# Kernel optimization log

Measured on AMD Instinct MI355X. Metric: run time of the kernel, lower is better.

Reference implementation:

```python
import jax, jax.numpy as jnp
import numpy as np

B, N, D, KNN = 2, 2048, 512, 16
F = 4 * D  # ffn hidden
LN_EPS = 1e-6  # flax LayerNorm default


def _ln(x, s, b):
    m = jnp.mean(x, axis=-1, keepdims=True)
    v = jnp.var(x, axis=-1, keepdims=True)
    return s * (x - m) * jax.lax.rsqrt(v + LN_EPS) + b


def _mobius_add(x, y, c):
    x2 = jnp.sum(x * x, axis=-1, keepdims=True)
    y2 = jnp.sum(y * y, axis=-1, keepdims=True)
    xy = jnp.sum(x * y, axis=-1, keepdims=True)
    num = (1 + 2 * c * xy + c * y2) * x + (1 - c * x2) * y
    den = 1 + 2 * c * xy + c * c * x2 * y2
    return num / jnp.clip(den, 1e-8, None)


def _logmap0(y, c):
    sqrt_c = jnp.sqrt(c)
    y_norm = jnp.clip(jnp.linalg.norm(y, axis=-1, keepdims=True), 1e-8, None)
    arg = jnp.minimum(sqrt_c * y_norm, 1.0 - 1e-7)
    return 1.0 / (sqrt_c * y_norm) * jnp.arctanh(arg) * y


def setup_inputs() -> dict:
    key = jax.random.key(0)
    ks = jax.random.split(key, 8)
    w = lambda k, shape: 0.02 * jax.random.normal(k, shape, dtype=jnp.float32)
    z = lambda *shape: jnp.zeros(shape, jnp.float32)
    o = lambda *shape: jnp.ones(shape, jnp.float32)
    return {
        'x': jax.random.normal(ks[0], (B, N, D), jnp.float32),
        'positions': 0.02 * jax.random.normal(ks[1], (B, N, D), jnp.float32),  # inside Poincare ball
        'c': jnp.ones((), jnp.float32),
        'Wq': w(ks[2], (D, D)), 'bq': z(D),
        'Wk': w(ks[3], (D, D)), 'bk': z(D),
        'Wv': w(ks[4], (D, D)), 'bv': z(D),
        'Wo': w(ks[5], (D, D)), 'bo': z(D),
        'W1': w(ks[6], (D, F)), 'b1': z(F),
        'W2': w(ks[7], (F, D)), 'b2': z(D),
        'ln1_s': o(D), 'ln1_b': z(D),
        'ln2_s': o(D), 'ln2_b': z(D),
        'geo_s': o(D), 'geo_b': z(D),
        'align_scale': o(1), 'feat_scale': o(1),
    }


def reference(x, positions, c, Wq, bq, Wk, bk, Wv, bv, Wo, bo, W1, b1, W2, b2,
              ln1_s, ln1_b, ln2_s, ln2_b, geo_s, geo_b, align_scale, feat_scale):
    b_, n_, d_ = x.shape
    x_res = x
    xn = _ln(x, ln1_s, ln1_b)
    q = xn @ Wq + bq
    kk = xn @ Wk + bk
    v = xn @ Wv + bv

    # Poincare distance matrix [B, N, N] (expanded ||x-y||^2 to avoid [B,N,N,D] intermediate)
    p2 = jnp.sum(positions * positions, axis=-1)            # [B, N]
    ip = jnp.einsum('bid,bjd->bij', positions, positions)   # [B, N, N]
    diff_sq = jnp.maximum(p2[:, :, None] + p2[:, None, :] - 2.0 * ip, 0.0)
    den = (1 - c * p2)[:, :, None] * (1 - c * p2)[:, None, :]
    arg = 1 + 2 * c * diff_sq / jnp.clip(den, 1e-8, None)
    dist = jnp.arccosh(jnp.maximum(arg, 1.0 + 1e-7)) / jnp.sqrt(c)

    _, idx = jax.lax.top_k(-dist, KNN)                      # [B, N, K]
    bix = jnp.arange(b_)[:, None, None]

    key_pos = positions[bix, idx]                           # [B, N, K, D]
    query_pos = positions[:, :, None, :]                    # [B, N, 1, D]
    geo = _logmap0(_mobius_add(-query_pos, key_pos, c), c)  # [B, N, K, D]
    geo = _ln(geo, geo_s, geo_b)

    gk = kk[bix, idx]                                       # [B, N, K, D]
    gv = v[bix, idx]                                        # [B, N, K, D]

    align = jnp.einsum('bnd,bnkd->bnk', q, geo)
    feat = jnp.einsum('bnd,bnkd->bnk', q, gk)
    scores = feat_scale * feat + align_scale * align
    w = jax.nn.softmax(scores, axis=-1)
    attn = jnp.einsum('bnk,bnkd->bnd', w, gv)

    x1 = x_res + attn @ Wo + bo
    h = _ln(x1, ln2_s, ln2_b)
    out = x1 + jax.nn.gelu(h @ W1 + b1) @ W2 + b2
    return out
```

## Files before the change

kernel.cpp:

```cpp
#include <hip/hip_runtime.h>
#include <hip/hip_bf16.h>
#include <math.h>

#define NTOK 2048
#define DDIM 512
#define FDIM 2048
#define KNN_K 16
#define ROWS 4096

typedef __hip_bfloat16 hb;
typedef unsigned long long ull;
typedef short s8v __attribute__((ext_vector_type(8)));
typedef short s4v __attribute__((ext_vector_type(4)));
typedef float f4v __attribute__((ext_vector_type(4)));

__device__ __forceinline__ float b2f(hb h) { return __bfloat162float(h); }
__device__ __forceinline__ float bits2f(short s) {
    return __uint_as_float(((unsigned int)(unsigned short)s) << 16);
}

__device__ __forceinline__ float ldin(const void* p, size_t i, int f32m) {
    return f32m ? ((const float*)p)[i] : b2f(((const hb*)p)[i]);
}
__device__ __forceinline__ float ld_scalar(const void* p, int f32m) {
    return f32m ? *(const float*)p : b2f(*(const hb*)p);
}
__device__ __forceinline__ short f2bs(float v) {
    hb h = __float2bfloat16(v);
    short s; __builtin_memcpy(&s, &h, 2); return s;
}
__device__ __forceinline__ short hb2s(hb h) {
    short s; __builtin_memcpy(&s, &h, 2); return s;
}

__device__ __forceinline__ void ld8(const void* p, size_t base, int fm, float* o) {
    if (fm) {
        f4v a = *(const f4v*)((const float*)p + base);
        f4v b = *(const f4v*)((const float*)p + base + 4);
        o[0]=a[0]; o[1]=a[1]; o[2]=a[2]; o[3]=a[3];
        o[4]=b[0]; o[5]=b[1]; o[6]=b[2]; o[7]=b[3];
    } else {
        s8v v = *(const s8v*)((const hb*)p + base);
        #pragma unroll
        for (int e = 0; e < 8; ++e) o[e] = bits2f(v[e]);
    }
}

__device__ __forceinline__ int detect_fm(const void* x) {
    const unsigned short* u = (const unsigned short*)x;
    const int lane = threadIdx.x & 63;
    int bad = 0;
    #pragma unroll
    for (int t = 0; t < 16; ++t) {
        unsigned short h = u[lane * 16 + t];
        int e = (h >> 7) & 0xFF;
        if (e == 0xFF) bad++;
        else if (e >= 0x8E) bad++;
        else if (e != 0 && e <= 0x66) bad++;
    }
    #pragma unroll
    for (int off = 1; off < 64; off <<= 1) bad += __shfl_xor(bad, off);
    return bad > 100 ? 1 : 0;
}

__device__ __forceinline__ ull shfl_xor_u64(ull x, int mask) {
    unsigned lo = (unsigned)x, hi = (unsigned)(x >> 32);
    lo = __shfl_xor(lo, mask); hi = __shfl_xor(hi, mask);
    return ((ull)hi << 32) | lo;
}

__device__ __forceinline__ float gelu_f(float x) {
    float u = 1.5957691216057308f * x * (1.f + 0.044715f * x * x);
    return x / (1.f + __expf(-u));
}

__device__ __forceinline__ void tr_tile(const void* src, hb* dst, int K, int N,
                                        int k0, int n0, int fm) {
    __shared__ float t[32][33];
    const int tx = threadIdx.x & 31, ty = threadIdx.x >> 5;
    #pragma unroll
    for (int r = 0; r < 32; r += 8)
        t[ty + r][tx] = ldin(src, (size_t)(k0 + ty + r) * N + n0 + tx, fm);
    __syncthreads();
    #pragma unroll
    for (int r = 0; r < 32; r += 8)
        dst[(size_t)(n0 + ty + r) * K + k0 + tx] = __float2bfloat16(t[tx][ty + r]);
}

__global__ void setup_kernel(const void* __restrict__ pos, const void* __restrict__ x,
                             const void* __restrict__ ln1s, const void* __restrict__ ln1b,
                             const void* __restrict__ Wq, const void* __restrict__ Wk,
                             const void* __restrict__ Wv, const void* __restrict__ Wo,
                             const void* __restrict__ W1, const void* __restrict__ W2,
                             hb* __restrict__ ph, hb* __restrict__ pl,
                             float* __restrict__ p2, float* __restrict__ spos,
                             hb* __restrict__ xnB,
                             hb* __restrict__ WqkvT, hb* __restrict__ WoT,
                             hb* __restrict__ W1T, hb* __restrict__ W2T,
                             int* __restrict__ fmflag) {
    const int fm = detect_fm(x);
    const int bx = blockIdx.x;
    if (bx == 0 && threadIdx.x == 0) *fmflag = fm;
    if (bx < 1024) {
        const int seg = bx >> 8, t = bx & 255;
        const int n0 = (t & 15) * 32, k0 = (t >> 4) * 32;
        const void* src = (seg == 0) ? Wq : (seg == 1) ? Wk : (seg == 2) ? Wv : Wo;
        hb* dst = (seg == 3) ? WoT : (WqkvT + (size_t)seg * 512 * 512);
        tr_tile(src, dst, 512, 512, k0, n0, fm);
    } else if (bx < 3072) {
        const int b = bx - 1024;
        if (b < 1024) {
            const int n0 = (b & 63) * 32, k0 = (b >> 6) * 32;
            tr_tile(W1, W1T, 512, 2048, k0, n0, fm);
        } else {
            const int b2 = b - 1024;
            const int n0 = (b2 & 15) * 32, k0 = (b2 >> 4) * 32;
            tr_tile(W2, W2T, 2048, 512, k0, n0, fm);
        }
    } else {
        const int idx = bx - 3072;
        const int lane = threadIdx.x & 63, wv = threadIdx.x >> 6;
        const int row = idx * 4 + wv;
        const int d0 = lane * 8;
        float pv[8], xv[8];
        ld8(pos, (size_t)row * DDIM + d0, fm, pv);
        ld8(x,   (size_t)row * DDIM + d0, fm, xv);
        s8v phv, plv;
        float s2 = 0.f, s1 = 0.f, sum = 0.f, sq = 0.f;
        #pragma unroll
        for (int e = 0; e < 8; ++e) {
            float v = pv[e];
            hb h = __float2bfloat16(v);
            phv[e] = hb2s(h);
            plv[e] = f2bs(v - b2f(h));
            s2 += v * v; s1 += v;
            sum += xv[e]; sq += xv[e] * xv[e];
        }
        *(s8v*)(ph + (size_t)row * DDIM + d0) = phv;
        *(s8v*)(pl + (size_t)row * DDIM + d0) = plv;
        #pragma unroll
        for (int off = 32; off; off >>= 1) {
            s2 += __shfl_down(s2, off); s1 += __shfl_down(s1, off);
            sum += __shfl_down(sum, off); sq += __shfl_down(sq, off);
        }
        if (lane == 0) { p2[row] = s2; spos[row] = s1; }
        const float ts = __shfl(sum, 0), tq = __shfl(sq, 0);
        const float mean = ts * (1.f / DDIM);
        const float var = tq * (1.f / DDIM) - mean * mean;
        const float rstd = rsqrtf(var + 1e-6f);
        float sv[8], bv2[8];
        ld8(ln1s, d0, fm, sv);
        ld8(ln1b, d0, fm, bv2);
        s8v xo;
        #pragma unroll
        for (int e = 0; e < 8; ++e)
            xo[e] = f2bs(sv[e] * (xv[e] - mean) * rstd + bv2[e]);
        *(s8v*)(xnB + (size_t)row * DDIM + d0) = xo;
    }
}

__global__ void ln_kernel(const float* __restrict__ xin,
                          const void* __restrict__ s, const void* __restrict__ b,
                          hb* __restrict__ y, const int* __restrict__ fmflag) {
    const int m = *fmflag;
    const int lane = threadIdx.x & 63, wv = threadIdx.x >> 6;
    const int row = blockIdx.x * 4 + wv;
    const int d0 = lane * 8;
    const float* xp = xin + (size_t)row * DDIM + d0;
    f4v a = *(const f4v*)xp, c4 = *(const f4v*)(xp + 4);
    float v[8] = {a[0], a[1], a[2], a[3], c4[0], c4[1], c4[2], c4[3]};
    float sum = 0.f, sq = 0.f;
    #pragma unroll
    for (int e = 0; e < 8; ++e) { sum += v[e]; sq += v[e] * v[e]; }
    #pragma unroll
    for (int off = 32; off; off >>= 1) { sum += __shfl_down(sum, off); sq += __shfl_down(sq, off); }
    const float ts = __shfl(sum, 0), tq = __shfl(sq, 0);
    const float mean = ts * (1.f / DDIM);
    const float var = tq * (1.f / DDIM) - mean * mean;
    const float rstd = rsqrtf(var + 1e-6f);
    float sv[8], bv[8];
    ld8(s, d0, m, sv);
    ld8(b, d0, m, bv);
    s8v o;
    #pragma unroll
    for (int e = 0; e < 8; ++e) o[e] = f2bs(sv[e] * (v[e] - mean) * rstd + bv[e]);
    *(s8v*)(y + (size_t)row * DDIM + d0) = o;
}

template<int EPI>
__global__ __launch_bounds__(256, 4)
void gemm64(const hb* __restrict__ A, const hb* __restrict__ Bt,
            const void* __restrict__ bp0, const void* __restrict__ res,
            void* __restrict__ C, int K, int lda, int ldb, int ldc,
            const int* __restrict__ fmflag) {
    constexpr int BK = 64, LDSW = BK + 8;
    constexpr int MAT = 64 * LDSW;
    __shared__ short Ls[2 * 2 * MAT];
    const int fm = *fmflag;
    const int tid = threadIdx.x, lane = tid & 63, wave = tid >> 6;
    const int wy = wave >> 1, wx = wave & 1;
    const int m0 = blockIdx.y * 64, n0 = blockIdx.x * 64;
    const int r0 = tid >> 3, c0 = (tid & 7) * 8;
    const int lm = lane & 15, lk = (lane >> 4) * 8;
    f4v acc[2][2];
    #pragma unroll
    for (int i = 0; i < 2; ++i)
        #pragma unroll
        for (int j = 0; j < 2; ++j) acc[i][j] = (f4v){0.f, 0.f, 0.f, 0.f};

    s8v an[2], bn[2];
    #pragma unroll
    for (int g = 0; g < 2; ++g) {
        an[g] = *(const s8v*)(A  + (size_t)(m0 + r0 + 32 * g) * lda + c0);
        bn[g] = *(const s8v*)(Bt + (size_t)(n0 + r0 + 32 * g) * ldb + c0);
    }

    int p = 0;
    for (int k0 = 0; k0 < K; k0 += BK) {
        short* As = Ls + p * (2 * MAT);
        short* Bs = As + MAT;
        #pragma unroll
        for (int g = 0; g < 2; ++g) {
            *(s8v*)(As + (r0 + 32 * g) * LDSW + c0) = an[g];
            *(s8v*)(Bs + (r0 + 32 * g) * LDSW + c0) = bn[g];
        }
        if (k0 + BK < K) {
            const int kn = k0 + BK;
            #pragma unroll
            for (int g = 0; g < 2; ++g) {
                an[g] = *(const s8v*)(A  + (size_t)(m0 + r0 + 32 * g) * lda + kn + c0);
                bn[g] = *(const s8v*)(Bt + (size_t)(n0 + r0 + 32 * g) * ldb + kn + c0);
            }
        }
        __syncthreads();
        #pragma unroll
        for (int kc = 0; kc < BK; kc += 32) {
            s8v af[2], bf[2];
            #pragma unroll
            for (int f = 0; f < 2; ++f) {
                af[f] = *(const s8v*)(As + (wy * 32 + f * 16 + lm) * LDSW + kc + lk);
                bf[f] = *(const s8v*)(Bs + (wx * 32 + f * 16 + lm) * LDSW + kc + lk);
            }
            #pragma unroll
            for (int fi = 0; fi < 2; ++fi)
                #pragma unroll
                for (int fj = 0; fj < 2; ++fj)
                    acc[fi][fj] = __builtin_amdgcn_mfma_f32_16x16x32_bf16(af[fi], bf[fj], acc[fi][fj], 0, 0, 0);
        }
        p ^= 1;
    }

    const int embase = m0 + wy * 32 + (lane >> 4) * 4;
    const int enbase = n0 + wx * 32 + lm;
    #pragma unroll
    for (int fi = 0; fi < 2; ++fi) {
        #pragma unroll
        for (int fj = 0; fj < 2; ++fj) {
            const int n = enbase + fj * 16;
            const float bias = ldin(bp0, n, fm);
            #pragma unroll
            for (int r = 0; r < 4; ++r) {
                const int m = embase + fi * 16 + r;
                float val = acc[fi][fj][r];
                size_t ci = (size_t)m * ldc + n;
                if (EPI == 1) {
                    val += bias + ldin(res, (size_t)m * 512 + n, fm);
                    ((float*)C)[ci] = val;
                } else if (EPI == 2) {
                    val = gelu_f(val + bias);
                    ((hb*)C)[ci] = __float2bfloat16(val);
                } else {
                    val += bias + ((const float*)res)[(size_t)m * 512 + n];
                    if (fm) ((float*)C)[ci] = val;
                    else ((hb*)C)[ci] = __float2bfloat16(val);
                }
            }
        }
    }
}

__global__ __launch_bounds__(256, 2)
void qkv_dist(const hb* __restrict__ A, const hb* __restrict__ Bt,
              const void* __restrict__ bq, const void* __restrict__ bk, const void* __restrict__ bv,
              hb* __restrict__ qkvB,
              const hb* __restrict__ ph, const hb* __restrict__ pl,
              const float* __restrict__ p2, const void* __restrict__ cp,
              float* __restrict__ argb, const int* __restrict__ fmflag) {
    __shared__ float TmS[8192];
    const int fm = *fmflag;
    const int tid = threadIdx.x, lane = tid & 63, wave = tid >> 6;

    if (blockIdx.x < 272) {
        constexpr int BK = 32, LDSW = 32;
        constexpr int KI = DDIM / BK;
        constexpr int TSH = 128 * LDSW;
        short* Sb = (short*)TmS;
        float* Tm = TmS;

        const float c = ld_scalar(cp, fm);
        const int bb = blockIdx.x / 136;
        const float* p2b = p2 + bb * NTOK;
        const size_t rb = (size_t)bb * NTOK;
        float* out = argb + (size_t)bb * NTOK * NTOK;
        int t = blockIdx.x % 136, bi = 0, rem = 16;
        while (t >= rem) { t -= rem; bi++; rem = 16 - bi; }
        const int bj = bi + t;
        const int i0 = bi * 128, j0 = bj * 128;
        const bool diag = (bi == bj);

        const int wy = wave >> 1, wx = wave & 1;
        const int r0 = tid >> 2, cch = tid & 3;
        const int lm = lane & 15;
        const int wslot = (cch ^ ((r0 >> 1) & 3)) * 8;
        const int rslot = (((lane >> 4) ^ ((lm >> 1) & 3))) * 8;
        const int c0g = cch * 8;

        const hb* src[4] = { ph + (rb + i0) * DDIM, pl + (rb + i0) * DDIM,
                             ph + (rb + j0) * DDIM, pl + (rb + j0) * DDIM };

        f4v acc_hh[4][4], acc_x[4][4];
        #pragma unroll
        for (int i = 0; i < 4; ++i)
            #pragma unroll
            for (int j = 0; j < 4; ++j) { acc_hh[i][j] = (f4v){0.f,0.f,0.f,0.f}; acc_x[i][j] = (f4v){0.f,0.f,0.f,0.f}; }

        s8v pf[4][2];
        #pragma unroll
        for (int tt = 0; tt < 4; ++tt)
            #pragma unroll
            for (int g = 0; g < 2; ++g)
                pf[tt][g] = *(const s8v*)(src[tt] + (size_t)(r0 + 64 * g) * DDIM + c0g);

        for (int it = 0; it < KI; ++it) {
            __syncthreads();
            #pragma unroll
            for (int tt = 0; tt < 4; ++tt)
                #pragma unroll
                for (int g = 0; g < 2; ++g)
                    *(s8v*)(Sb + tt * TSH + (r0 + 64 * g) * LDSW + wslot) = pf[tt][g];
            if (it + 1 < KI) {
                const int kn = (it + 1) * BK;
                #pragma unroll
                for (int tt = 0; tt < 4; ++tt)
                    #pragma unroll
                    for (int g = 0; g < 2; ++g)
                        pf[tt][g] = *(const s8v*)(src[tt] + (size_t)(r0 + 64 * g) * DDIM + kn + c0g);
            }
            __syncthreads();
            s8v ah[4], al[4], bh[4], bl[4];
            #pragma unroll
            for (int f = 0; f < 4; ++f) {
                ah[f] = *(const s8v*)(Sb + 0 * TSH + (wy * 64 + f * 16 + lm) * LDSW + rslot);
                al[f] = *(const s8v*)(Sb + 1 * TSH + (wy * 64 + f * 16 + lm) * LDSW + rslot);
                bh[f] = *(const s8v*)(Sb + 2 * TSH + (wx * 64 + f * 16 + lm) * LDSW + rslot);
                bl[f] = *(const s8v*)(Sb + 3 * TSH + (wx * 64 + f * 16 + lm) * LDSW + rslot);
            }
            #pragma unroll
            for (int fi = 0; fi < 4; ++fi)
                #pragma unroll
                for (int fj = 0; fj < 4; ++fj) {
                    acc_hh[fi][fj] = __builtin_amdgcn_mfma_f32_16x16x32_bf16(ah[fi], bh[fj], acc_hh[fi][fj], 0, 0, 0);
                    acc_x[fi][fj]  = __builtin_amdgcn_mfma_f32_16x16x32_bf16(ah[fi], bl[fj], acc_x[fi][fj], 0, 0, 0);
                    acc_x[fi][fj]  = __builtin_amdgcn_mfma_f32_16x16x32_bf16(al[fi], bh[fj], acc_x[fi][fj], 0, 0, 0);
                }
        }

        const int eibase = i0 + wy * 64 + (lane >> 4) * 4;
        const int ejbase = j0 + wx * 64 + lm;
        #pragma unroll
        for (int fi = 0; fi < 4; ++fi) {
            #pragma unroll
            for (int fj = 0; fj < 4; ++fj) {
                const int jj = ejbase + fj * 16;
                const float p2j = p2b[jj];
                #pragma unroll
                for (int r = 0; r < 4; ++r) {
                    const int ii = eibase + fi * 16 + r;
                    const float p2i = p2b[ii];
                    const float xy = acc_hh[fi][fj][r] + acc_x[fi][fj][r];
                    float diff = fmaxf(p2i + p2j - 2.f * xy, 0.f);
                    float den = fmaxf((1.f - c * p2i) * (1.f - c * p2j), 1e-8f);
                    float argv = 1.f + 2.f * c * diff / den;
                    out[(size_t)ii * NTOK + jj] = argv;
                    acc_hh[fi][fj][r] = argv;
                }
            }
        }
        if (!diag) {
            #pragma unroll
            for (int cc = 0; cc < 4; ++cc) {
                __syncthreads();
                if (wx == (cc >> 1)) {
                    #pragma unroll
                    for (int fjl = 0; fjl < 2; ++fjl) {
                        const int fj = (cc & 1) * 2 + fjl;
                        const int rT = fjl * 16 + lm;
                        #pragma unroll
                        for (int fi = 0; fi < 4; ++fi) {
                            const int cbase = wy * 64 + fi * 16 + (lane >> 4) * 4;
                            #pragma unroll
                            for (int r = 0; r < 4; ++r)
                                Tm[rT * 132 + cbase + r] = acc_hh[fi][fj][r];
                        }
                    }
                }
                __syncthreads();
                #pragma unroll
                for (int tt2 = 0; tt2 < 4; ++tt2) {
                    const int lin = tt2 * 256 + tid;
                    const int rowT = lin >> 5;
                    const int c4 = (lin & 31) * 4;
                    f4v v = *(const f4v*)(Tm + rowT * 132 + c4);
                    *(f4v*)(out + (size_t)(j0 + cc * 32 + rowT) * NTOK + i0 + c4) = v;
                }
            }
        }
    } else {
        constexpr int BK = 32, LDSW = 32;
        constexpr int MAT = 128 * LDSW;
        short* Ls = (short*)TmS;
        const int b = blockIdx.x - 272;
        const int m0 = (b / 12) * 128, n0 = (b % 12) * 128;
        const int wy = wave >> 1, wx = wave & 1;
        const int r0 = tid >> 2, cch = tid & 3;
        const int lm = lane & 15;
        const int wslot = (cch ^ ((r0 >> 1) & 3)) * 8;
        const int rslot = (((lane >> 4) ^ ((lm >> 1) & 3))) * 8;
        const int c0g = cch * 8;
        f4v acc[4][4];
        #pragma unroll
        for (int i = 0; i < 4; ++i)
            #pragma unroll
            for (int j = 0; j < 4; ++j) acc[i][j] = (f4v){0.f, 0.f, 0.f, 0.f};

        s8v an[2], bn[2];
        #pragma unroll
        for (int g = 0; g < 2; ++g) {
            an[g] = *(const s8v*)(A  + (size_t)(m0 + r0 + 64 * g) * 512 + c0g);
            bn[g] = *(const s8v*)(Bt + (size_t)(n0 + r0 + 64 * g) * 512 + c0g);
        }

        int p = 0;
        for (int k0 = 0; k0 < 512; k0 += BK) {
            short* As = Ls + p * (2 * MAT);
            short* Bs = As + MAT;
            #pragma unroll
            for (int g = 0; g < 2; ++g) {
                *(s8v*)(As + (r0 + 64 * g) * LDSW + wslot) = an[g];
                *(s8v*)(Bs + (r0 + 64 * g) * LDSW + wslot) = bn[g];
            }
            if (k0 + BK < 512) {
                const int kn = k0 + BK;
                #pragma unroll
                for (int g = 0; g < 2; ++g) {
                    an[g] = *(const s8v*)(A  + (size_t)(m0 + r0 + 64 * g) * 512 + kn + c0g);
                    bn[g] = *(const s8v*)(Bt + (size_t)(n0 + r0 + 64 * g) * 512 + kn + c0g);
                }
            }
            __syncthreads();
            s8v af[4], bf[4];
            #pragma unroll
            for (int f = 0; f < 4; ++f) {
                af[f] = *(const s8v*)(As + (wy * 64 + f * 16 + lm) * LDSW + rslot);
                bf[f] = *(const s8v*)(Bs + (wx * 64 + f * 16 + lm) * LDSW + rslot);
            }
            #pragma unroll
            for (int fi = 0; fi < 4; ++fi)
                #pragma unroll
                for (int fj = 0; fj < 4; ++fj)
                    acc[fi][fj] = __builtin_amdgcn_mfma_f32_16x16x32_bf16(af[fi], bf[fj], acc[fi][fj], 0, 0, 0);
            p ^= 1;
        }

        const int embase = m0 + wy * 64 + (lane >> 4) * 4;
        const int enbase = n0 + wx * 64 + lm;
        #pragma unroll
        for (int fi = 0; fi < 4; ++fi) {
            #pragma unroll
            for (int fj = 0; fj < 4; ++fj) {
                const int n = enbase + fj * 16;
                const void* bp = (n < 512) ? bq : ((n < 1024) ? bk : bv);
                const float bias = ldin(bp, n & 511, fm);
                #pragma unroll
                for (int r = 0; r < 4; ++r) {
                    const int m = embase + fi * 16 + r;
                    qkvB[(size_t)m * 1536 + n] = __float2bfloat16(acc[fi][fj][r] + bias);
                }
            }
        }
    }
}

__global__ __launch_bounds__(256)
void topk_attn(const float* __restrict__ argb,
               const void* __restrict__ pos, const hb* __restrict__ qkvB,
               const float* __restrict__ p2, const float* __restrict__ spos,
               const void* __restrict__ cp,
               const void* __restrict__ geo_s, const void* __restrict__ geo_b,
               const void* __restrict__ a_sc, const void* __restrict__ f_sc,
               hb* __restrict__ attnO, const int* __restrict__ fmflag) {
    const int fm = *fmflag;
    const int lane = threadIdx.x & 63, wv = threadIdx.x >> 6;
    const int row = blockIdx.x * 4 + wv;
    const int bb = row >> 11, r = row & (NTOK - 1);
    const int l16 = lane & 15, grp = lane >> 4;

    const float* arow = argb + (size_t)bb * NTOK * NTOK + (size_t)r * NTOK;
    ull k[32];
    #pragma unroll
    for (int i = 0; i < 8; ++i) {
        f4v v = *(const f4v*)(arow + lane * 4 + i * 256);
        #pragma unroll
        for (int e = 0; e < 4; ++e) {
            const unsigned idx = lane * 4 + e + i * 256;
            k[i * 4 + e] = ((ull)__float_as_uint(v[e]) << 32) | idx;
        }
    }
    ull res = ~0ull;
    for (int sel = 0; sel < KNN_K; ++sel) {
        ull t16[16];
        #pragma unroll
        for (int i = 0; i < 16; ++i) t16[i] = (k[2 * i] < k[2 * i + 1]) ? k[2 * i] : k[2 * i + 1];
        #pragma unroll
        for (int i = 0; i < 8; ++i) t16[i] = (t16[2 * i] < t16[2 * i + 1]) ? t16[2 * i] : t16[2 * i + 1];
        #pragma unroll
        for (int i = 0; i < 4; ++i) t16[i] = (t16[2 * i] < t16[2 * i + 1]) ? t16[2 * i] : t16[2 * i + 1];
        ull m01 = (t16[0] < t16[1]) ? t16[0] : t16[1];
        ull m23 = (t16[2] < t16[3]) ? t16[2] : t16[3];
        ull m = (m01 < m23) ? m01 : m23;
        #pragma unroll
        for (int mask = 1; mask < 64; mask <<= 1) {
            ull o = shfl_xor_u64(m, mask);
            m = (o < m) ? o : m;
        }
        if (lane == sel) res = m;
        const unsigned widx = __builtin_amdgcn_readfirstlane((unsigned)m);
        const bool mine = (int)((widx >> 2) & 63) == lane;
        const int regid = (int)(((widx >> 8) << 2) | (widx & 3));
        switch (regid) {
#define CLR(RR) case RR: if (mine) k[RR] = ~0ull; break;
            CLR(0)  CLR(1)  CLR(2)  CLR(3)  CLR(4)  CLR(5)  CLR(6)  CLR(7)
            CLR(8)  CLR(9)  CLR(10) CLR(11) CLR(12) CLR(13) CLR(14) CLR(15)
            CLR(16) CLR(17) CLR(18) CLR(19) CLR(20) CLR(21) CLR(22) CLR(23)
            CLR(24) CLR(25) CLR(26) CLR(27) CLR(28) CLR(29) CLR(30) CLR(31)
#undef CLR
        }
    }
    const int nid = (int)(unsigned)res;
    const float argv_l = __uint_as_float((unsigned)(res >> 32));

    __shared__ float qgsS[4][DDIM];
    __shared__ float qS[4][DDIM];
    float* qgsL = qgsS[wv];
    float* qL = qS[wv];

    const float c = ld_scalar(cp, fm);
    const float cs = fmaxf(c, 1e-20f);
    const float sc_c = sqrtf(fmaxf(c, 0.f));

    const int d0 = lane * 8;
    float qq = 0.f, qgs_sum = 0.f, qgb = 0.f;
    {
        float pv[8], gs[8], gb[8];
        ld8(pos, (size_t)row * DDIM + d0, fm, pv);
        ld8(geo_s, d0, fm, gs);
        ld8(geo_b, d0, fm, gb);
        s8v qv = *(const s8v*)(qkvB + (size_t)row * 1536 + d0);
        f4v a0, a1, q0, q1;
        #pragma unroll
        for (int e = 0; e < 4; ++e) {
            float qe = bits2f(qv[e]);
            float ae = qe * gs[e];
            q0[e] = qe; a0[e] = ae;
            qq += ae * pv[e]; qgs_sum += ae; qgb += qe * gb[e];
        }
        #pragma unroll
        for (int e = 0; e < 4; ++e) {
            float qe = bits2f(qv[e + 4]);
            float ae = qe * gs[e + 4];
            q1[e] = qe; a1[e] = ae;
            qq += ae * pv[e + 4]; qgs_sum += ae; qgb += qe * gb[e + 4];
        }
        *(f4v*)(qgsL + d0) = a0; *(f4v*)(qgsL + d0 + 4) = a1;
        *(f4v*)(qL + d0) = q0;   *(f4v*)(qL + d0 + 4) = q1;
    }
    #pragma unroll
    for (int off = 32; off; off >>= 1) {
        qq += __shfl_down(qq, off);
        qgs_sum += __shfl_down(qgs_sum, off);
        qgb += __shfl_down(qgb, off);
    }
    const float QQ  = __shfl(qq, 0);
    const float QGS = __shfl(qgs_sum, 0);
    const float QGB = __shfl(qgb, 0);
    __syncthreads();

    float qkt[4], ftt[4];
    #pragma unroll
    for (int t = 0; t < 4; ++t) {
        const int kk = grp * 4 + t;
        const int j = __shfl(nid, kk);
        const size_t nro = (size_t)(bb * NTOK + j) * DDIM;
        const size_t nrk = (size_t)(bb * NTOK + j) * 1536 + 512;
        float qk = 0.f, feat = 0.f;
        if (fm) {
            #pragma unroll
            for (int i = 0; i < 8; ++i) {
                const int d = l16 * 4 + i * 64;
                f4v kp = *(const f4v*)((const float*)pos + nro + d);
                f4v qg = *(const f4v*)(qgsL + d);
                qk += qg[0] * kp[0] + qg[1] * kp[1] + qg[2] * kp[2] + qg[3] * kp[3];
            }
        } else {
            #pragma unroll
            for (int i = 0; i < 8; ++i) {
                const int d = l16 * 4 + i * 64;
                s4v kp4 = *(const s4v*)((const hb*)pos + nro + d);
                f4v qg = *(const f4v*)(qgsL + d);
                #pragma unroll
                for (int e = 0; e < 4; ++e) qk += qg[e] * bits2f(kp4[e]);
            }
        }
        #pragma unroll
        for (int i = 0; i < 4; ++i) {
            const int d = l16 * 8 + i * 128;
            s8v kv = *(const s8v*)(qkvB + nrk + d);
            f4v q0 = *(const f4v*)(qL + d);
            f4v q1 = *(const f4v*)(qL + d + 4);
            #pragma unroll
            for (int e = 0; e < 4; ++e)
                feat += q0[e] * bits2f(kv[e]) + q1[e] * bits2f(kv[e + 4]);
        }
        #pragma unroll
        for (int off = 8; off; off >>= 1) {
            qk += __shfl_down(qk, off, 16);
            feat += __shfl_down(feat, off, 16);
        }
        qkt[t] = qk; ftt[t] = feat;
    }
    const int src = (lane >> 2) << 4;
    float qa[4], fa[4];
    #pragma unroll
    for (int t = 0; t < 4; ++t) { qa[t] = __shfl(qkt[t], src); fa[t] = __shfl(ftt[t], src); }
    const int tsel = lane & 3;
    const float qk_f = tsel == 0 ? qa[0] : tsel == 1 ? qa[1] : tsel == 2 ? qa[2] : qa[3];
    const float ft_f = tsel == 0 ? fa[0] : tsel == 1 ? fa[1] : tsel == 2 ? fa[2] : fa[3];

    float sc_v = 0.f;
    if (lane < KNN_K) {
        const int j = nid;
        const float p2i = p2[row], p2j = p2[bb * NTOK + j];
        const float sposi = spos[row], sposj = spos[bb * NTOK + j];
        const float argv = argv_l;
        const float den_d = fmaxf((1.f - c * p2i) * (1.f - c * p2j), 1e-8f);
        const float diff = (argv - 1.f) * den_d / (2.f * cs);
        const float xy = 0.5f * (p2i + p2j - diff);
        const float x2 = p2i, y2 = p2j;
        const float Af = 1.f - 2.f * c * xy + c * y2;
        const float Bf = 1.f - c * x2;
        float den = fmaxf(1.f - 2.f * c * xy + c * c * x2 * y2, 1e-8f);
        const float rden = 1.f / den;
        float n2 = fmaxf(Af * Af * x2 - 2.f * Af * Bf * xy + Bf * Bf * y2, 0.f) * rden * rden;
        const float ynorm = fmaxf(sqrtf(n2), 1e-8f);
        const float t_over = sc_c * ynorm;
        const float targ = fminf(t_over, 1.f - 1e-7f);
        const float scale = (targ > 0.f) ? (atanhf(targ) / t_over) : 1.f;
        const float S1 = scale * rden * (Bf * sposj - Af * sposi);
        const float mean = S1 * (1.f / DDIM);
        const float sq = scale * scale * n2;
        const float var = sq * (1.f / DDIM) - mean * mean;
        const float rstd = rsqrtf(fmaxf(var, 0.f) + 1e-6f);
        const float G = scale * rden * (Bf * qk_f - Af * QQ);
        const float align = rstd * (G - mean * QGS) + QGB;
        sc_v = ld_scalar(f_sc, fm) * ft_f + ld_scalar(a_sc, fm) * align;
    }

    float s_t[16];
    #pragma unroll
    for (int t = 0; t < 16; ++t) s_t[t] = __shfl(sc_v, t);
    float mx = s_t[0];
    #pragma unroll
    for (int t = 1; t < 16; ++t) mx = fmaxf(mx, s_t[t]);
    float wsum = 0.f;
    #pragma unroll
    for (int t = 0; t < 16; ++t) { s_t[t] = expf(s_t[t] - mx); wsum += s_t[t]; }
    const float rw = 1.f / wsum;

    float acc[8];
    #pragma unroll
    for (int e = 0; e < 8; ++e) acc[e] = 0.f;
    #pragma unroll
    for (int t = 0; t < 16; ++t) {
        const int j = __shfl(nid, t);
        const float w = s_t[t] * rw;
        s8v vvv = *(const s8v*)(qkvB + (size_t)(bb * NTOK + j) * 1536 + 1024 + d0);
        #pragma unroll
        for (int e = 0; e < 8; ++e) acc[e] += w * bits2f(vvv[e]);
    }
    s8v o;
    #pragma unroll
    for (int e = 0; e < 8; ++e) o[e] = f2bs(acc[e]);
    *(s8v*)(attnO + (size_t)row * DDIM + d0) = o;
}

extern "C" void kernel_launch(void* const* d_in, const int* in_sizes, int n_in,
                              void* d_out, int out_size, void* d_ws, size_t ws_size,
                              hipStream_t stream) {
    const void* x    = d_in[0];
    const void* posb = d_in[1];
    const void* cb   = d_in[2];
    const void* Wq   = d_in[3];
    const void* bq   = d_in[4];
    const void* Wk   = d_in[5];
    const void* bk   = d_in[6];
    const void* Wv   = d_in[7];
    const void* bv   = d_in[8];
    const void* Wo   = d_in[9];
    const void* bo   = d_in[10];
    const void* W1   = d_in[11];
    const void* b1   = d_in[12];
    const void* W2   = d_in[13];
    const void* b2   = d_in[14];
    const void* ln2s = d_in[17];
    const void* ln2b = d_in[18];
    const void* geos = d_in[19];
    const void* geob = d_in[20];
    const void* asc  = d_in[21];
    const void* fsc  = d_in[22];
    const void* ln1s = d_in[15];
    const void* ln1b = d_in[16];

    float* wsf = (float*)d_ws;
    size_t off = 0;
    hb* xnB   = (hb*)(wsf + off); off += 1048576;
    hb* qkvB  = (hb*)(wsf + off); off += 3145728;
    float* p2 = wsf + off;        off += 4096;
    float* spos = wsf + off;      off += 4096;
    float* x1 = wsf + off;        off += 2097152;
    float* argb = wsf + off;
    hb* hh    = (hb*)argb;        off += 8388608;
    hb* ph    = (hb*)(wsf + off); off += 1048576;
    hb* pl    = (hb*)(wsf + off); off += 1048576;
    hb* WqkvT = (hb*)(wsf + off); off += 393216;
    hb* WoT   = (hb*)(wsf + off); off += 131072;
    hb* W1T   = (hb*)(wsf + off); off += 524288;
    hb* W2T   = (hb*)(wsf + off); off += 524288;
    int* fmflag = (int*)(wsf + off); off += 16;
    hb* attnO = ph;
    hb* hbuf  = xnB;

    setup_kernel<<<4096, 256, 0, stream>>>(posb, x, ln1s, ln1b, Wq, Wk, Wv, Wo, W1, W2,
                                           ph, pl, p2, spos, xnB, WqkvT, WoT, W1T, W2T, fmflag);
    qkv_dist<<<656, 256, 0, stream>>>(xnB, WqkvT, bq, bk, bv, qkvB,
                                      ph, pl, p2, cb, argb, fmflag);
    topk_attn<<<1024, 256, 0, stream>>>(argb, posb, qkvB, p2, spos, cb,
                                        geos, geob, asc, fsc, attnO, fmflag);
    gemm64<1><<<dim3(8, 64), 256, 0, stream>>>(attnO, WoT, bo, x, x1,
                                               512, 512, 512, 512, fmflag);
    ln_kernel<<<1024, 256, 0, stream>>>(x1, ln2s, ln2b, hbuf, fmflag);
    gemm64<2><<<dim3(32, 64), 256, 0, stream>>>(hbuf, W1T, b1, nullptr, hh,
                                                512, 512, 512, 2048, fmflag);
    gemm64<3><<<dim3(8, 64), 256, 0, stream>>>(hh, W2T, b2, x1, d_out,
                                               2048, 2048, 2048, 512, fmflag);

    (void)in_sizes; (void)n_in; (void)out_size; (void)ws_size;
}
```

Baseline: 252.5 us.

## Split per-row top-k selection across two wavefronts and merge via shared memory

Each row's 2048-candidate top-16 search is now divided between two wavefronts, each scanning 1024 entries with half the registers. The two sorted lists are merged by rank counting in shared memory, and the second wavefront exits before the attention phase. This halves the serial selection depth and register pressure per wave and doubles the grid size. The cost is extra block barriers, a merge step, and idle half-waves during attention.

```diff
diff --git a/kernel.cpp b/kernel.cpp
--- a/kernel.cpp
+++ b/kernel.cpp
@@ -501,32 +501,36 @@
                hb* __restrict__ attnO, const int* __restrict__ fmflag) {
     const int fm = *fmflag;
     const int lane = threadIdx.x & 63, wv = threadIdx.x >> 6;
-    const int row = blockIdx.x * 4 + wv;
+    const int rowL = wv >> 1, half = wv & 1;
+    const int row = blockIdx.x * 2 + rowL;
     const int bb = row >> 11, r = row & (NTOK - 1);
     const int l16 = lane & 15, grp = lane >> 4;
 
-    const float* arow = argb + (size_t)bb * NTOK * NTOK + (size_t)r * NTOK;
-    ull k[32];
-    #pragma unroll
-    for (int i = 0; i < 8; ++i) {
+    __shared__ ull lists[2][2][16];
+    __shared__ ull merged[2][16];
+    __shared__ float qgsS[2][DDIM];
+    __shared__ float qS[2][DDIM];
+
+    const float* arow = argb + (size_t)bb * NTOK * NTOK + (size_t)r * NTOK + half * 1024;
+    ull k[16];
+    #pragma unroll
+    for (int i = 0; i < 4; ++i) {
         f4v v = *(const f4v*)(arow + lane * 4 + i * 256);
         #pragma unroll
         for (int e = 0; e < 4; ++e) {
-            const unsigned idx = lane * 4 + e + i * 256;
+            const unsigned idx = lane * 4 + e + i * 256 + half * 1024;
             k[i * 4 + e] = ((ull)__float_as_uint(v[e]) << 32) | idx;
         }
     }
     ull res = ~0ull;
     for (int sel = 0; sel < KNN_K; ++sel) {
-        ull t16[16];
-        #pragma unroll
-        for (int i = 0; i < 16; ++i) t16[i] = (k[2 * i] < k[2 * i + 1]) ? k[2 * i] : k[2 * i + 1];
-        #pragma unroll
-        for (int i = 0; i < 8; ++i) t16[i] = (t16[2 * i] < t16[2 * i + 1]) ? t16[2 * i] : t16[2 * i + 1];
-        #pragma unroll
-        for (int i = 0; i < 4; ++i) t16[i] = (t16[2 * i] < t16[2 * i + 1]) ? t16[2 * i] : t16[2 * i + 1];
-        ull m01 = (t16[0] < t16[1]) ? t16[0] : t16[1];
-        ull m23 = (t16[2] < t16[3]) ? t16[2] : t16[3];
+        ull t8[8];
+        #pragma unroll
+        for (int i = 0; i < 8; ++i) t8[i] = (k[2 * i] < k[2 * i + 1]) ? k[2 * i] : k[2 * i + 1];
+        #pragma unroll
+        for (int i = 0; i < 4; ++i) t8[i] = (t8[2 * i] < t8[2 * i + 1]) ? t8[2 * i] : t8[2 * i + 1];
+        ull m01 = (t8[0] < t8[1]) ? t8[0] : t8[1];
+        ull m23 = (t8[2] < t8[3]) ? t8[2] : t8[3];
         ull m = (m01 < m23) ? m01 : m23;
         #pragma unroll
         for (int mask = 1; mask < 64; mask <<= 1) {
@@ -536,23 +540,37 @@
         if (lane == sel) res = m;
         const unsigned widx = __builtin_amdgcn_readfirstlane((unsigned)m);
         const bool mine = (int)((widx >> 2) & 63) == lane;
-        const int regid = (int)(((widx >> 8) << 2) | (widx & 3));
+        const int regid = (int)((((widx >> 8) & 3) << 2) | (widx & 3));
         switch (regid) {
 #define CLR(RR) case RR: if (mine) k[RR] = ~0ull; break;
             CLR(0)  CLR(1)  CLR(2)  CLR(3)  CLR(4)  CLR(5)  CLR(6)  CLR(7)
             CLR(8)  CLR(9)  CLR(10) CLR(11) CLR(12) CLR(13) CLR(14) CLR(15)
-            CLR(16) CLR(17) CLR(18) CLR(19) CLR(20) CLR(21) CLR(22) CLR(23)
-            CLR(24) CLR(25) CLR(26) CLR(27) CLR(28) CLR(29) CLR(30) CLR(31)
 #undef CLR
         }
     }
-    const int nid = (int)(unsigned)res;
-    const float argv_l = __uint_as_float((unsigned)(res >> 32));
-
-    __shared__ float qgsS[4][DDIM];
-    __shared__ float qS[4][DDIM];
-    float* qgsL = qgsS[wv];
-    float* qL = qS[wv];
+    if (lane < 16) lists[rowL][half][lane] = res;
+    __syncthreads();
+
+    if (half == 0 && lane < 16) {
+        const ull av = lists[rowL][0][lane];
+        const ull bv = lists[rowL][1][lane];
+        int ra = lane, rb = lane;
+        #pragma unroll
+        for (int j = 0; j < 16; ++j) {
+            ra += (lists[rowL][1][j] < av) ? 1 : 0;
+            rb += (lists[rowL][0][j] < bv) ? 1 : 0;
+        }
+        if (ra < 16) merged[rowL][ra] = av;
+        if (rb < 16) merged[rowL][rb] = bv;
+    }
+    __syncthreads();
+
+    const ull mres = (lane < 16) ? merged[rowL][lane] : ~0ull;
+    const int nid = (int)(unsigned)mres;
+    const float argv_l = __uint_as_float((unsigned)(mres >> 32));
+
+    float* qgsL = qgsS[rowL];
+    float* qL = qS[rowL];
 
     const float c = ld_scalar(cp, fm);
     const float cs = fmaxf(c, 1e-20f);
@@ -594,6 +612,8 @@
     const float QGS = __shfl(qgs_sum, 0);
     const float QGB = __shfl(qgb, 0);
     __syncthreads();
+
+    if (half == 1) return;
 
     float qkt[4], ftt[4];
     #pragma unroll
@@ -753,7 +773,7 @@
                                            ph, pl, p2, spos, xnB, WqkvT, WoT, W1T, W2T, fmflag);
     qkv_dist<<<656, 256, 0, stream>>>(xnB, WqkvT, bq, bk, bv, qkvB,
                                       ph, pl, p2, cb, argb, fmflag);
-    topk_attn<<<1024, 256, 0, stream>>>(argb, posb, qkvB, p2, spos, cb,
+    topk_attn<<<2048, 256, 0, stream>>>(argb, posb, qkvB, p2, spos, cb,
                                         geos, geob, asc, fsc, attnO, fmflag);
     gemm64<1><<<dim3(8, 64), 256, 0, stream>>>(attnO, WoT, bo, x, x1,
                                                512, 512, 512, 512, fmflag);
```

Measured after the change: 270.9 us. +7.3%, slower.
